# Kernel tuning notes

Measured on AMD Instinct MI355X. Metric: run time of the kernel, lower is better.

Reference implementation:

```python
import jax, jax.numpy as jnp
import numpy as np

N_HEAD = 8
LN_EPS = 1e-5


def _ln(z, g, b):
    m = jnp.mean(z, axis=-1, keepdims=True)
    v = jnp.var(z, axis=-1, keepdims=True)
    return (z - m) / jnp.sqrt(v + LN_EPS) * g + b


def setup_inputs() -> dict:
    key = jax.random.key(0)
    ks = jax.random.split(key, 20)
    B, N, H, F = 4, 256, 128, 512
    p = {}
    p["x"] = jax.random.normal(ks[0], (B, N, H), dtype=jnp.float32)
    p["e"] = jax.random.normal(ks[1], (B, N, N, H), dtype=jnp.float32)
    p["attention_mask"] = jnp.zeros((B, N_HEAD, N, N), dtype=jnp.float32)
    s = 0.02
    p["Wq"] = jax.random.normal(ks[2], (H, H)) * s; p["bq"] = jnp.zeros((H,))
    p["Wk"] = jax.random.normal(ks[3], (H, H)) * s; p["bk"] = jnp.zeros((H,))
    p["Wv"] = jax.random.normal(ks[4], (H, H)) * s; p["bv"] = jnp.zeros((H,))
    p["We"] = jax.random.normal(ks[5], (H, H)) * s; p["be"] = jnp.zeros((H,))
    p["Woh"] = jax.random.normal(ks[6], (H, H)) * s; p["boh"] = jnp.zeros((H,))
    p["Woe"] = jax.random.normal(ks[7], (H, H)) * s; p["boe"] = jnp.zeros((H,))
    p["Wf1x"] = jax.random.normal(ks[8], (H, F)) * s; p["bf1x"] = jnp.zeros((F,))
    p["Wf2x"] = jax.random.normal(ks[9], (F, H)) * s; p["bf2x"] = jnp.zeros((H,))
    p["Wf1e"] = jax.random.normal(ks[10], (H, F)) * s; p["bf1e"] = jnp.zeros((F,))
    p["Wf2e"] = jax.random.normal(ks[11], (F, H)) * s; p["bf2e"] = jnp.zeros((H,))
    p["g1x"] = jnp.ones((H,)); p["b1x"] = jnp.zeros((H,))
    p["g1e"] = jnp.ones((H,)); p["b1e"] = jnp.zeros((H,))
    return p


def reference(x, e, attention_mask, Wq, bq, Wk, bk, Wv, bv, We, be,
              Woh, boh, Woe, boe, Wf1x, bf1x, Wf2x, bf2x,
              Wf1e, bf1e, Wf2e, bf2e, g1x, b1x, g1e, b1e):
    B, N, H = x.shape
    h = N_HEAD
    d = H // h
    # projections; NOTE: V uses the K projection (faithful to original bug)
    Qx = (x @ Wq + bq).reshape(B, N, h, d).transpose(0, 2, 1, 3)   # (B,h,N,d)
    Kx = (x @ Wk + bk).reshape(B, N, h, d).transpose(0, 2, 1, 3)
    Vx = (x @ Wk + bk).reshape(B, N, h, d).transpose(0, 2, 1, 3)
    Ee = (e @ We + be).reshape(B, N, N, h, d).transpose(0, 3, 1, 2, 4)  # (B,h,N,N,d)
    scale = 1.0 / np.sqrt(d).astype(np.float32)
    inter = Qx[:, :, :, None, :] * Kx[:, :, None, :, :] * Ee * scale   # (B,h,N,N,d)
    scores = jax.nn.softmax(attention_mask + inter.sum(-1), axis=-1)   # (B,h,N,N)
    e_attn = inter.transpose(0, 2, 3, 1, 4).reshape(B, N, N, H) @ Woe + boe
    att = jnp.einsum('bhij,bhjd->bhid', scores, Vx)
    x_attn = att.transpose(0, 2, 1, 3).reshape(B, N, H) @ Woh + boh
    # residual + layernorm (original 'layer' path reuses normalization1_* twice)
    x1 = _ln(x_attn + x, g1x, b1x)
    e1 = _ln(e_attn + e, g1e, b1e)
    x_ff = jax.nn.relu(x1 @ Wf1x + bf1x) @ Wf2x + bf2x
    e_ff = jax.nn.relu(e1 @ Wf1e + bf1e) @ Wf2e + bf2e
    x2 = _ln(x_ff + x1, g1x, b1x)
    e2 = _ln(e_ff + e1, g1e, b1e)
    return x2, e2
```

## Files before the change

kernel.cpp:

```cpp
#include <hip/hip_runtime.h>
#include <math.h>

#define NSEQ 256
#define HD 128
#define FD 512
#define NHD 8
#define LNEPS 1e-5f

typedef __attribute__((ext_vector_type(8))) short bf16x8;
typedef __attribute__((ext_vector_type(4))) float f32x4;

__device__ __forceinline__ unsigned short f2bf(float x) {
  union { float f; unsigned int u; } v; v.f = x;
  unsigned int r = v.u + 0x7fffu + ((v.u >> 16) & 1u);
  return (unsigned short)(r >> 16);
}

__device__ __forceinline__ float bf2f(unsigned short u) {
  union { float f; unsigned int v; } cv; cv.v = ((unsigned int)u) << 16;
  return cv.f;
}

__global__ void prep_weights(
    const float* __restrict__ W1x, const float* __restrict__ W2x,
    const float* __restrict__ W1e, const float* __restrict__ W2e,
    unsigned short* __restrict__ W1Tx, unsigned short* __restrict__ W2Tx,
    unsigned short* __restrict__ W1Fe, unsigned short* __restrict__ W2Fe) {
  int t = blockIdx.x * 256 + threadIdx.x;
  int tot = gridDim.x * 256;
  for (int idx = t; idx < FD * HD; idx += tot) {
    int n = idx >> 7, k = idx & (HD - 1);
    float v = W1x[k * FD + n];
    W1Tx[idx] = f2bf(v);
    float ve = W1e[k * FD + n];
    int dst = ((((n >> 4) * 4 + (k >> 5)) * 64) + ((k >> 3) & 3) * 16 + (n & 15)) * 8 + (k & 7);
    W1Fe[dst] = f2bf(ve);
  }
  for (int idx = t; idx < HD * FD; idx += tot) {
    int n = idx >> 9, k = idx & (FD - 1);
    float v = W2x[k * HD + n];
    W2Tx[idx] = f2bf(v);
    float ve = W2e[k * HD + n];
    int dst = ((((n >> 4) * 16 + (k >> 5)) * 64) + ((k >> 3) & 3) * 16 + (n & 15)) * 8 + (k & 7);
    W2Fe[dst] = f2bf(ve);
  }
}

__global__ __launch_bounds__(128) void qk_proj(const float* __restrict__ x,
    const float* __restrict__ Wq, const float* __restrict__ bq,
    const float* __restrict__ Wk, const float* __restrict__ bk,
    float* __restrict__ Qs, float* __restrict__ Kp) {
  int row = blockIdx.x;
  int c = threadIdx.x;
  __shared__ float xl[HD];
  xl[c] = x[row * HD + c];
  __syncthreads();
  float aq = bq[c], ak = bk[c];
  #pragma unroll 8
  for (int k = 0; k < HD; ++k) {
    float xv = xl[k];
    aq = fmaf(xv, Wq[k * HD + c], aq);
    ak = fmaf(xv, Wk[k * HD + c], ak);
  }
  Qs[row * HD + c] = aq * 0.25f;
  Kp[row * HD + c] = ak;
}

__global__ __launch_bounds__(256) void edge_attn(
    const float* __restrict__ e,
    const float* __restrict__ We, const float* __restrict__ be,
    const float* __restrict__ Woe, const float* __restrict__ boe,
    const float* __restrict__ Qs, const float* __restrict__ Kp,
    const float* __restrict__ g1e, const float* __restrict__ b1e,
    float* __restrict__ Sout, float* __restrict__ e1out) {
  const int gid = blockIdx.x;
  const int jt = gid & 3, i = (gid >> 2) & (NSEQ - 1), b = gid >> 10;
  const int j0 = jt * 64;
  const int t = threadIdx.x;
  const int w = t >> 6, l = t & 63;
  const int wr = w >> 1, wc = w & 1;
  const int l15 = l & 15, lg = l >> 4;

  __shared__ unsigned short eL[64 * 128];
  __shared__ unsigned short kL[64 * 136];
  __shared__ float qL[HD], beL[HD], boeL[HD], gL[HD], bbL[HD];
  __shared__ float redS[64][2], redQ[64][2];

  if (t < HD) {
    qL[t]   = Qs[(b * NSEQ + i) * HD + t];
    beL[t]  = be[t];
    boeL[t] = boe[t];
    gL[t]   = g1e[t];
    bbL[t]  = b1e[t];
  }
  const int ebase = ((b * NSEQ + i) * NSEQ + j0) * HD;
  for (int v = t; v < 64 * 16; v += 256) {
    int r = v >> 4, c8 = (v & 15) << 3;
    const float* se = &e[ebase + r * HD + c8];
    float4 e0 = *(const float4*)se;
    float4 e1v = *(const float4*)(se + 4);
    union { bf16x8 v8; unsigned short u[8]; } pk;
    pk.u[0] = f2bf(e0.x); pk.u[1] = f2bf(e0.y); pk.u[2] = f2bf(e0.z); pk.u[3] = f2bf(e0.w);
    pk.u[4] = f2bf(e1v.x); pk.u[5] = f2bf(e1v.y); pk.u[6] = f2bf(e1v.z); pk.u[7] = f2bf(e1v.w);
    *(bf16x8*)&eL[r * HD + (c8 ^ ((r & 7) << 3))] = pk.v8;
    const float* sk = &Kp[(b * NSEQ + j0 + r) * HD + c8];
    float4 k0 = *(const float4*)sk;
    float4 k1 = *(const float4*)(sk + 4);
    pk.u[0] = f2bf(k0.x); pk.u[1] = f2bf(k0.y); pk.u[2] = f2bf(k0.z); pk.u[3] = f2bf(k0.w);
    pk.u[4] = f2bf(k1.x); pk.u[5] = f2bf(k1.y); pk.u[6] = f2bf(k1.z); pk.u[7] = f2bf(k1.w);
    *(bf16x8*)&kL[r * 136 + c8] = pk.v8;
  }
  __syncthreads();

  f32x4 acc1[2][4];
  #pragma unroll
  for (int tm = 0; tm < 2; ++tm)
    #pragma unroll
    for (int tn = 0; tn < 4; ++tn) {
      float bv = beL[wc * 64 + tn * 16 + l15];
      acc1[tm][tn] = (f32x4){bv, bv, bv, bv};
    }
  #pragma unroll
  for (int ks = 0; ks < 4; ++ks) {
    bf16x8 af[2], bfr[4];
    #pragma unroll
    for (int tm = 0; tm < 2; ++tm) {
      int mrow = wr * 32 + tm * 16 + l15;
      af[tm] = *(const bf16x8*)&eL[mrow * HD + ((ks * 32 + lg * 8) ^ ((mrow & 7) << 3))];
    }
    #pragma unroll
    for (int tn = 0; tn < 4; ++tn) {
      int n = wc * 64 + tn * 16 + l15;
      const float* wp = &We[(ks * 32 + lg * 8) * HD + n];
      union { bf16x8 v8; unsigned short u[8]; } pk;
      #pragma unroll
      for (int ii = 0; ii < 8; ++ii) pk.u[ii] = f2bf(wp[ii * HD]);
      bfr[tn] = pk.v8;
    }
    #pragma unroll
    for (int tm = 0; tm < 2; ++tm)
      #pragma unroll
      for (int tn = 0; tn < 4; ++tn)
        acc1[tm][tn] = __builtin_amdgcn_mfma_f32_16x16x32_bf16(af[tm], bfr[tn], acc1[tm][tn], 0, 0, 0);
  }

  #pragma unroll
  for (int tm = 0; tm < 2; ++tm)
    #pragma unroll
    for (int tn = 0; tn < 4; ++tn) {
      int c = wc * 64 + tn * 16 + l15;
      float qv = qL[c];
      f32x4 p;
      #pragma unroll
      for (int ii = 0; ii < 4; ++ii) {
        int r = wr * 32 + tm * 16 + lg * 4 + ii;
        p[ii] = acc1[tm][tn][ii] * qv * bf2f(kL[r * 136 + c]);
      }
      acc1[tm][tn] = p;
      float h0 = p[0], h1 = p[1], h2 = p[2], h3 = p[3];
      #pragma unroll
      for (int off = 1; off < 16; off <<= 1) {
        h0 += __shfl_xor(h0, off); h1 += __shfl_xor(h1, off);
        h2 += __shfl_xor(h2, off); h3 += __shfl_xor(h3, off);
      }
      if (l15 < 4) {
        float val = l15 == 0 ? h0 : l15 == 1 ? h1 : l15 == 2 ? h2 : h3;
        int r = wr * 32 + tm * 16 + lg * 4 + l15;
        Sout[((b * NHD + (wc * 4 + tn)) * NSEQ + i) * NSEQ + j0 + r] = val;
      }
    }
  __syncthreads();

  #pragma unroll
  for (int tm = 0; tm < 2; ++tm)
    #pragma unroll
    for (int tn = 0; tn < 4; ++tn) {
      int c = wc * 64 + tn * 16 + l15;
      #pragma unroll
      for (int ii = 0; ii < 4; ++ii) {
        int r = wr * 32 + tm * 16 + lg * 4 + ii;
        eL[r * HD + (c ^ ((r & 7) << 3))] = f2bf(acc1[tm][tn][ii]);
      }
    }
  __syncthreads();

  f32x4 acc2[2][4];
  #pragma unroll
  for (int tm = 0; tm < 2; ++tm)
    #pragma unroll
    for (int tn = 0; tn < 4; ++tn) {
      float bv = boeL[wc * 64 + tn * 16 + l15];
      acc2[tm][tn] = (f32x4){bv, bv, bv, bv};
    }
  #pragma unroll
  for (int ks = 0; ks < 4; ++ks) {
    bf16x8 af[2], bfr[4];
    #pragma unroll
    for (int tm = 0; tm < 2; ++tm) {
      int mrow = wr * 32 + tm * 16 + l15;
      af[tm] = *(const bf16x8*)&eL[mrow * HD + ((ks * 32 + lg * 8) ^ ((mrow & 7) << 3))];
    }
    #pragma unroll
    for (int tn = 0; tn < 4; ++tn) {
      int n = wc * 64 + tn * 16 + l15;
      const float* wp = &Woe[(ks * 32 + lg * 8) * HD + n];
      union { bf16x8 v8; unsigned short u[8]; } pk;
      #pragma unroll
      for (int ii = 0; ii < 8; ++ii) pk.u[ii] = f2bf(wp[ii * HD]);
      bfr[tn] = pk.v8;
    }
    #pragma unroll
    for (int tm = 0; tm < 2; ++tm)
      #pragma unroll
      for (int tn = 0; tn < 4; ++tn)
        acc2[tm][tn] = __builtin_amdgcn_mfma_f32_16x16x32_bf16(af[tm], bfr[tn], acc2[tm][tn], 0, 0, 0);
  }

  #pragma unroll
  for (int tm = 0; tm < 2; ++tm) {
    #pragma unroll
    for (int tn = 0; tn < 4; ++tn) {
      int c = wc * 64 + tn * 16 + l15;
      #pragma unroll
      for (int ii = 0; ii < 4; ++ii) {
        int r = wr * 32 + tm * 16 + lg * 4 + ii;
        acc2[tm][tn][ii] += e[ebase + r * HD + c];
      }
    }
    #pragma unroll
    for (int ii = 0; ii < 4; ++ii) {
      float s  = acc2[tm][0][ii] + acc2[tm][1][ii] + acc2[tm][2][ii] + acc2[tm][3][ii];
      float sq = acc2[tm][0][ii] * acc2[tm][0][ii] + acc2[tm][1][ii] * acc2[tm][1][ii]
               + acc2[tm][2][ii] * acc2[tm][2][ii] + acc2[tm][3][ii] * acc2[tm][3][ii];
      #pragma unroll
      for (int off = 1; off < 16; off <<= 1) {
        s += __shfl_xor(s, off); sq += __shfl_xor(sq, off);
      }
      if (l15 == 0) {
        int r = wr * 32 + tm * 16 + lg * 4 + ii;
        redS[r][wc] = s; redQ[r][wc] = sq;
      }
    }
  }
  __syncthreads();

  #pragma unroll
  for (int tm = 0; tm < 2; ++tm) {
    float mrow[4], rsrow[4];
    #pragma unroll
    for (int ii = 0; ii < 4; ++ii) {
      int r = wr * 32 + tm * 16 + lg * 4 + ii;
      float s = redS[r][0] + redS[r][1];
      float sq = redQ[r][0] + redQ[r][1];
      float m = s * (1.f / HD);
      float var = sq * (1.f / HD) - m * m;
      mrow[ii] = m; rsrow[ii] = rsqrtf(var + LNEPS);
    }
    #pragma unroll
    for (int tn = 0; tn < 4; ++tn) {
      int c = wc * 64 + tn * 16 + l15;
      float gv = gL[c], bv = bbL[c];
      #pragma unroll
      for (int ii = 0; ii < 4; ++ii) {
        int r = wr * 32 + tm * 16 + lg * 4 + ii;
        e1out[ebase + r * HD + c] = (acc2[tm][tn][ii] - mrow[ii]) * rsrow[ii] * gv + bv;
      }
    }
  }
}

__global__ __launch_bounds__(256) void softmax_k(float* __restrict__ S,
    const float* __restrict__ mask) {
  int row = blockIdx.x;
  int t = threadIdx.x;
  int idx = row * NSEQ + t;
  float v = S[idx] + mask[idx];
  float m = v;
  #pragma unroll
  for (int off = 1; off < 64; off <<= 1) m = fmaxf(m, __shfl_xor(m, off));
  __shared__ float wbuf[8];
  if ((t & 63) == 0) wbuf[t >> 6] = m;
  __syncthreads();
  m = fmaxf(fmaxf(wbuf[0], wbuf[1]), fmaxf(wbuf[2], wbuf[3]));
  float ex = __expf(v - m);
  float s = ex;
  #pragma unroll
  for (int off = 1; off < 64; off <<= 1) s += __shfl_xor(s, off);
  __syncthreads();
  if ((t & 63) == 0) wbuf[4 + (t >> 6)] = s;
  __syncthreads();
  s = wbuf[4] + wbuf[5] + wbuf[6] + wbuf[7];
  S[idx] = ex / s;
}

__global__ __launch_bounds__(128) void x_attn_ln(
    const float* __restrict__ x, const float* __restrict__ scores,
    const float* __restrict__ Kp,
    const float* __restrict__ Woh, const float* __restrict__ boh,
    const float* __restrict__ g1x, const float* __restrict__ b1x,
    float* __restrict__ x1out) {
  int bi = blockIdx.x; int b = bi >> 8; int i = bi & 255;
  int c = threadIdx.x;
  __shared__ float sL[NHD * NSEQ];
  __shared__ float attL[HD];
  __shared__ float rbuf[4];

  for (int v = c; v < NHD * NSEQ; v += 128) {
    int h = v >> 8, j = v & 255;
    sL[v] = scores[((b * NHD + h) * NSEQ + i) * NSEQ + j];
  }
  __syncthreads();
  int h = c >> 4;
  float att = 0.f;
  for (int j = 0; j < NSEQ; ++j)
    att = fmaf(sL[h * NSEQ + j], Kp[(b * NSEQ + j) * HD + c], att);
  attL[c] = att;
  __syncthreads();
  float o = boh[c];
  for (int k = 0; k < HD; ++k) o = fmaf(attL[k], Woh[k * HD + c], o);
  o += x[bi * HD + c];
  float s = o, s2 = o * o;
  #pragma unroll
  for (int off = 1; off < 64; off <<= 1) { s += __shfl_xor(s, off); s2 += __shfl_xor(s2, off); }
  if ((c & 63) == 0) { rbuf[(c >> 6) * 2] = s; rbuf[(c >> 6) * 2 + 1] = s2; }
  __syncthreads();
  s = rbuf[0] + rbuf[2]; s2 = rbuf[1] + rbuf[3];
  float m = s * (1.f / HD);
  float var = s2 * (1.f / HD) - m * m;
  x1out[bi * HD + c] = (o - m) * rsqrtf(var + LNEPS) * g1x[c] + b1x[c];
}

__global__ __launch_bounds__(256) void ffn_mfma(
    const float* in1,
    const unsigned short* __restrict__ W1T, const float* __restrict__ b1,
    const unsigned short* __restrict__ W2T, const float* __restrict__ b2,
    const float* __restrict__ g, const float* __restrict__ bb,
    float* out2) {
  const int row0 = blockIdx.x * 64;
  const int t = threadIdx.x;
  const int w = t >> 6, l = t & 63;
  const int wr = w >> 1, wc = w & 1;
  const int l15 = l & 15, lg = l >> 4;

  __shared__ __align__(16) char smem[34816];
  unsigned short* aL = (unsigned short*)smem;
  unsigned short* hL = (unsigned short*)(smem + 16384);
  float* b1L = (float*)(smem + 32768);
  float* epi = (float*)smem;

  for (int v = t; v < 64 * 16; v += 256) {
    int r = v >> 4, c8 = (v & 15) << 3;
    const float* src = &in1[(row0 + r) * HD + c8];
    float4 f0 = *(const float4*)src;
    float4 f1 = *(const float4*)(src + 4);
    union { bf16x8 v8; unsigned short u[8]; } pk;
    pk.u[0] = f2bf(f0.x); pk.u[1] = f2bf(f0.y); pk.u[2] = f2bf(f0.z); pk.u[3] = f2bf(f0.w);
    pk.u[4] = f2bf(f1.x); pk.u[5] = f2bf(f1.y); pk.u[6] = f2bf(f1.z); pk.u[7] = f2bf(f1.w);
    *(bf16x8*)&aL[r * HD + (c8 ^ ((r & 7) << 3))] = pk.v8;
  }
  for (int v = t; v < FD; v += 256) b1L[v] = b1[v];
  __syncthreads();

  f32x4 acc2[2][4];
  #pragma unroll
  for (int tm = 0; tm < 2; ++tm)
    #pragma unroll
    for (int tn = 0; tn < 4; ++tn) acc2[tm][tn] = (f32x4){0.f, 0.f, 0.f, 0.f};

  for (int fc = 0; fc < 4; ++fc) {
    f32x4 acc1[2][4];
    #pragma unroll
    for (int tm = 0; tm < 2; ++tm)
      #pragma unroll
      for (int tn = 0; tn < 4; ++tn) acc1[tm][tn] = (f32x4){0.f, 0.f, 0.f, 0.f};
    #pragma unroll
    for (int ks = 0; ks < 4; ++ks) {
      bf16x8 af[2], bfr[4];
      #pragma unroll
      for (int tm = 0; tm < 2; ++tm) {
        int mrow = wr * 32 + tm * 16 + l15;
        af[tm] = *(const bf16x8*)&aL[mrow * HD + ((ks * 32 + lg * 8) ^ ((mrow & 7) << 3))];
      }
      #pragma unroll
      for (int tn = 0; tn < 4; ++tn) {
        int n = fc * 128 + wc * 64 + tn * 16 + l15;
        bfr[tn] = *(const bf16x8*)&W1T[n * HD + ks * 32 + lg * 8];
      }
      #pragma unroll
      for (int tm = 0; tm < 2; ++tm)
        #pragma unroll
        for (int tn = 0; tn < 4; ++tn)
          acc1[tm][tn] = __builtin_amdgcn_mfma_f32_16x16x32_bf16(af[tm], bfr[tn], acc1[tm][tn], 0, 0, 0);
    }
    __syncthreads();
    #pragma unroll
    for (int tm = 0; tm < 2; ++tm)
      #pragma unroll
      for (int tn = 0; tn < 4; ++tn) {
        int col = wc * 64 + tn * 16 + l15;
        float bias = b1L[fc * 128 + col];
        #pragma unroll
        for (int ii = 0; ii < 4; ++ii) {
          int r = wr * 32 + tm * 16 + lg * 4 + ii;
          float hv = fmaxf(acc1[tm][tn][ii] + bias, 0.f);
          hL[r * HD + (col ^ ((r & 7) << 3))] = f2bf(hv);
        }
      }
    __syncthreads();
    #pragma unroll
    for (int ks = 0; ks < 4; ++ks) {
      bf16x8 af[2], bfr[4];
      #pragma unroll
      for (int tm = 0; tm < 2; ++tm) {
        int mrow = wr * 32 + tm * 16 + l15;
        af[tm] = *(const bf16x8*)&hL[mrow * HD + ((ks * 32 + lg * 8) ^ ((mrow & 7) << 3))];
      }
      #pragma unroll
      for (int tn = 0; tn < 4; ++tn) {
        int n = wc * 64 + tn * 16 + l15;
        bfr[tn] = *(const bf16x8*)&W2T[n * FD + fc * 128 + ks * 32 + lg * 8];
      }
      #pragma unroll
      for (int tm = 0; tm < 2; ++tm)
        #pragma unroll
        for (int tn = 0; tn < 4; ++tn)
          acc2[tm][tn] = __builtin_amdgcn_mfma_f32_16x16x32_bf16(af[tm], bfr[tn], acc2[tm][tn], 0, 0, 0);
    }
  }

  float res[2][4][4];
  #pragma unroll
  for (int tm = 0; tm < 2; ++tm)
    #pragma unroll
    for (int tn = 0; tn < 4; ++tn) {
      int col = wc * 64 + tn * 16 + l15;
      #pragma unroll
      for (int ii = 0; ii < 4; ++ii) {
        int r = wr * 32 + tm * 16 + lg * 4 + ii;
        res[tm][tn][ii] = bf2f(aL[r * HD + (col ^ ((r & 7) << 3))]);
      }
    }
  __syncthreads();

  #pragma unroll
  for (int tm = 0; tm < 2; ++tm)
    #pragma unroll
    for (int tn = 0; tn < 4; ++tn) {
      int col = wc * 64 + tn * 16 + l15;
      float bias = b2[col];
      #pragma unroll
      for (int ii = 0; ii < 4; ++ii) {
        int r = wr * 32 + tm * 16 + lg * 4 + ii;
        epi[r * 132 + col] = acc2[tm][tn][ii] + bias + res[tm][tn][ii];
      }
    }
  __syncthreads();
  {
    int r = t >> 2, sgi = t & 3;
    const float* rowp = &epi[r * 132 + sgi * 32];
    float sum = 0.f, sq = 0.f;
    #pragma unroll
    for (int u = 0; u < 32; u += 4) {
      float4 v4 = *(const float4*)&rowp[u];
      sum += v4.x + v4.y + v4.z + v4.w;
      sq  += v4.x * v4.x + v4.y * v4.y + v4.z * v4.z + v4.w * v4.w;
    }
    sum += __shfl_xor(sum, 1); sq += __shfl_xor(sq, 1);
    sum += __shfl_xor(sum, 2); sq += __shfl_xor(sq, 2);
    float m = sum * (1.f / HD);
    float var = sq * (1.f / HD) - m * m;
    float rs = rsqrtf(var + LNEPS);
    #pragma unroll
    for (int u = 0; u < 32; u += 4) {
      float4 v4 = *(const float4*)&rowp[u];
      int cb = sgi * 32 + u;
      float4 o;
      o.x = (v4.x - m) * rs * g[cb + 0] + bb[cb + 0];
      o.y = (v4.y - m) * rs * g[cb + 1] + bb[cb + 1];
      o.z = (v4.z - m) * rs * g[cb + 2] + bb[cb + 2];
      o.w = (v4.w - m) * rs * g[cb + 3] + bb[cb + 3];
      *(float4*)&out2[(row0 + r) * HD + cb] = o;
    }
  }
}

__global__ __launch_bounds__(256) void ffn_mfma_e(
    const float* in1,
    const unsigned short* __restrict__ W1F, const float* __restrict__ b1,
    const unsigned short* __restrict__ W2F, const float* __restrict__ b2,
    const float* __restrict__ g, const float* __restrict__ bb,
    float* out2) {
  const int t = threadIdx.x;
  const int w = t >> 6, l = t & 63;
  const int wr = w >> 1, wc = w & 1;
  const int l15 = l & 15, lg = l >> 4;
  const int rowbase = blockIdx.x * 256;

  __shared__ __align__(16) char smem[35840];
  unsigned short* aL = (unsigned short*)smem;
  unsigned short* hL = (unsigned short*)(smem + 16384);
  float* b1L  = (float*)(smem + 32768);
  float* redS = (float*)(smem + 34816);
  float* redQ = (float*)(smem + 35328);

  for (int v = t; v < FD; v += 256) b1L[v] = b1[v];

  for (int ch = 0; ch < 4; ++ch) {
    const int row0 = rowbase + ch * 64;
    __syncthreads();

    for (int v = t; v < 64 * 16; v += 256) {
      int r = v >> 4, c8 = (v & 15) << 3;
      const float* src = &in1[(row0 + r) * HD + c8];
      float4 f0 = *(const float4*)src;
      float4 f1 = *(const float4*)(src + 4);
      union { bf16x8 v8; unsigned short u[8]; } pk;
      pk.u[0] = f2bf(f0.x); pk.u[1] = f2bf(f0.y); pk.u[2] = f2bf(f0.z); pk.u[3] = f2bf(f0.w);
      pk.u[4] = f2bf(f1.x); pk.u[5] = f2bf(f1.y); pk.u[6] = f2bf(f1.z); pk.u[7] = f2bf(f1.w);
      *(bf16x8*)&aL[r * HD + (c8 ^ ((r & 7) << 3))] = pk.v8;
    }
    __syncthreads();

    f32x4 acc2[2][4];
    #pragma unroll
    for (int tm = 0; tm < 2; ++tm)
      #pragma unroll
      for (int tn = 0; tn < 4; ++tn) acc2[tm][tn] = (f32x4){0.f, 0.f, 0.f, 0.f};

    for (int fc = 0; fc < 4; ++fc) {
      f32x4 acc1[2][4];
      #pragma unroll
      for (int tm = 0; tm < 2; ++tm)
        #pragma unroll
        for (int tn = 0; tn < 4; ++tn) acc1[tm][tn] = (f32x4){0.f, 0.f, 0.f, 0.f};
      #pragma unroll
      for (int ks = 0; ks < 4; ++ks) {
        bf16x8 af[2], bfr[4];
        #pragma unroll
        for (int tm = 0; tm < 2; ++tm) {
          int mrow = wr * 32 + tm * 16 + l15;
          af[tm] = *(const bf16x8*)&aL[mrow * HD + ((ks * 32 + lg * 8) ^ ((mrow & 7) << 3))];
        }
        #pragma unroll
        for (int tn = 0; tn < 4; ++tn) {
          int nt = fc * 8 + wc * 4 + tn;
          bfr[tn] = *(const bf16x8*)&W1F[(((nt * 4 + ks) * 64) + l) * 8];
        }
        #pragma unroll
        for (int tm = 0; tm < 2; ++tm)
          #pragma unroll
          for (int tn = 0; tn < 4; ++tn)
            acc1[tm][tn] = __builtin_amdgcn_mfma_f32_16x16x32_bf16(af[tm], bfr[tn], acc1[tm][tn], 0, 0, 0);
      }
      __syncthreads();
      #pragma unroll
      for (int tm = 0; tm < 2; ++tm)
        #pragma unroll
        for (int tn = 0; tn < 4; ++tn) {
          int col = wc * 64 + tn * 16 + l15;
          float bias = b1L[fc * 128 + col];
          #pragma unroll
          for (int ii = 0; ii < 4; ++ii) {
            int r = wr * 32 + tm * 16 + lg * 4 + ii;
            float hv = fmaxf(acc1[tm][tn][ii] + bias, 0.f);
            hL[r * HD + (col ^ ((r & 7) << 3))] = f2bf(hv);
          }
        }
      __syncthreads();
      #pragma unroll
      for (int ks = 0; ks < 4; ++ks) {
        bf16x8 af[2], bfr[4];
        #pragma unroll
        for (int tm = 0; tm < 2; ++tm) {
          int mrow = wr * 32 + tm * 16 + l15;
          af[tm] = *(const bf16x8*)&hL[mrow * HD + ((ks * 32 + lg * 8) ^ ((mrow & 7) << 3))];
        }
        #pragma unroll
        for (int tn = 0; tn < 4; ++tn) {
          int nt = wc * 4 + tn;
          int ksg = fc * 4 + ks;
          bfr[tn] = *(const bf16x8*)&W2F[(((nt * 16 + ksg) * 64) + l) * 8];
        }
        #pragma unroll
        for (int tm = 0; tm < 2; ++tm)
          #pragma unroll
          for (int tn = 0; tn < 4; ++tn)
            acc2[tm][tn] = __builtin_amdgcn_mfma_f32_16x16x32_bf16(af[tm], bfr[tn], acc2[tm][tn], 0, 0, 0);
      }
    }

    #pragma unroll
    for (int tm = 0; tm < 2; ++tm) {
      #pragma unroll
      for (int tn = 0; tn < 4; ++tn) {
        int col = wc * 64 + tn * 16 + l15;
        float bias = b2[col];
        #pragma unroll
        for (int ii = 0; ii < 4; ++ii) {
          int r = wr * 32 + tm * 16 + lg * 4 + ii;
          acc2[tm][tn][ii] += bias + bf2f(aL[r * HD + (col ^ ((r & 7) << 3))]);
        }
      }
      #pragma unroll
      for (int ii = 0; ii < 4; ++ii) {
        float s  = acc2[tm][0][ii] + acc2[tm][1][ii] + acc2[tm][2][ii] + acc2[tm][3][ii];
        float sq = acc2[tm][0][ii] * acc2[tm][0][ii] + acc2[tm][1][ii] * acc2[tm][1][ii]
                 + acc2[tm][2][ii] * acc2[tm][2][ii] + acc2[tm][3][ii] * acc2[tm][3][ii];
        #pragma unroll
        for (int off = 1; off < 16; off <<= 1) {
          s += __shfl_xor(s, off); sq += __shfl_xor(sq, off);
        }
        if (l15 == 0) {
          int r = wr * 32 + tm * 16 + lg * 4 + ii;
          redS[r * 2 + wc] = s; redQ[r * 2 + wc] = sq;
        }
      }
    }
    __syncthreads();

    #pragma unroll
    for (int tm = 0; tm < 2; ++tm) {
      float mrow[4], rsrow[4];
      #pragma unroll
      for (int ii = 0; ii < 4; ++ii) {
        int r = wr * 32 + tm * 16 + lg * 4 + ii;
        float s = redS[r * 2] + redS[r * 2 + 1];
        float sq = redQ[r * 2] + redQ[r * 2 + 1];
        float m = s * (1.f / HD);
        float var = sq * (1.f / HD) - m * m;
        mrow[ii] = m; rsrow[ii] = rsqrtf(var + LNEPS);
      }
      #pragma unroll
      for (int tn = 0; tn < 4; ++tn) {
        int col = wc * 64 + tn * 16 + l15;
        float gv = g[col], bv = bb[col];
        #pragma unroll
        for (int ii = 0; ii < 4; ++ii) {
          int r = wr * 32 + tm * 16 + lg * 4 + ii;
          out2[(row0 + r) * HD + col] = (acc2[tm][tn][ii] - mrow[ii]) * rsrow[ii] * gv + bv;
        }
      }
    }
  }
}

extern "C" void kernel_launch(void* const* d_in, const int* in_sizes, int n_in,
                              void* d_out, int out_size, void* d_ws, size_t ws_size,
                              hipStream_t stream) {
  const float* x    = (const float*)d_in[0];
  const float* e    = (const float*)d_in[1];
  const float* mask = (const float*)d_in[2];
  const float* Wq   = (const float*)d_in[3];
  const float* bq   = (const float*)d_in[4];
  const float* Wk   = (const float*)d_in[5];
  const float* bk   = (const float*)d_in[6];
  const float* We   = (const float*)d_in[9];
  const float* be   = (const float*)d_in[10];
  const float* Woh  = (const float*)d_in[11];
  const float* boh  = (const float*)d_in[12];
  const float* Woe  = (const float*)d_in[13];
  const float* boe  = (const float*)d_in[14];
  const float* Wf1x = (const float*)d_in[15];
  const float* bf1x = (const float*)d_in[16];
  const float* Wf2x = (const float*)d_in[17];
  const float* bf2x = (const float*)d_in[18];
  const float* Wf1e = (const float*)d_in[19];
  const float* bf1e = (const float*)d_in[20];
  const float* Wf2e = (const float*)d_in[21];
  const float* bf2e = (const float*)d_in[22];
  const float* g1x  = (const float*)d_in[23];
  const float* b1x  = (const float*)d_in[24];
  const float* g1e  = (const float*)d_in[25];
  const float* b1e  = (const float*)d_in[26];

  float* xout = (float*)d_out;
  float* eout = (float*)d_out + 131072;

  char* ws = (char*)d_ws;
  unsigned short* W1Fe = (unsigned short*)(ws);
  unsigned short* W2Fe = (unsigned short*)(ws + 131072);
  unsigned short* W1Tx = (unsigned short*)(ws + 262144);
  unsigned short* W2Tx = (unsigned short*)(ws + 393216);
  float* Qs  = (float*)(ws + 524288);
  float* Kp  = (float*)(ws + 1048576);
  float* x1b = (float*)(ws + 1572864);
  float* S   = (float*)(ws + 2097152);

  prep_weights<<<64, 256, 0, stream>>>(Wf1x, Wf2x, Wf1e, Wf2e, W1Tx, W2Tx, W1Fe, W2Fe);
  qk_proj<<<1024, 128, 0, stream>>>(x, Wq, bq, Wk, bk, Qs, Kp);
  edge_attn<<<4096, 256, 0, stream>>>(e, We, be, Woe, boe, Qs, Kp, g1e, b1e, S, eout);
  softmax_k<<<8192, 256, 0, stream>>>(S, mask);
  x_attn_ln<<<1024, 128, 0, stream>>>(x, S, Kp, Woh, boh, g1x, b1x, x1b);
  ffn_mfma<<<16, 256, 0, stream>>>(x1b, W1Tx, bf1x, W2Tx, bf2x, g1x, b1x, xout);
  ffn_mfma_e<<<1024, 256, 0, stream>>>(eout, W1Fe, bf1e, W2Fe, bf2e, g1e, b1e, eout);
}
```

Before: 408.0 us.

## Fuse edge FFN and second layernorm into the edge attention kernel

The edge FFN (two bf16 MFMA GEMMs with ReLU, residual and layernorm) now runs inside the edge attention kernel. The e1 tile stays in LDS as bf16, and the K tile buffer is reused for the hidden activations. This removes one 64 MB write and one 64 MB read of the intermediate e1 tensor plus a separate launch. In exchange each block holds more LDS and registers, which may lower occupancy of the fused kernel.

```diff
diff --git a/kernel.cpp b/kernel.cpp
--- a/kernel.cpp
+++ b/kernel.cpp
@@ -30,16 +30,14 @@
   int tot = gridDim.x * 256;
   for (int idx = t; idx < FD * HD; idx += tot) {
     int n = idx >> 7, k = idx & (HD - 1);
-    float v = W1x[k * FD + n];
-    W1Tx[idx] = f2bf(v);
+    W1Tx[idx] = f2bf(W1x[k * FD + n]);
     float ve = W1e[k * FD + n];
     int dst = ((((n >> 4) * 4 + (k >> 5)) * 64) + ((k >> 3) & 3) * 16 + (n & 15)) * 8 + (k & 7);
     W1Fe[dst] = f2bf(ve);
   }
   for (int idx = t; idx < HD * FD; idx += tot) {
     int n = idx >> 9, k = idx & (FD - 1);
-    float v = W2x[k * HD + n];
-    W2Tx[idx] = f2bf(v);
+    W2Tx[idx] = f2bf(W2x[k * HD + n]);
     float ve = W2e[k * HD + n];
     int dst = ((((n >> 4) * 16 + (k >> 5)) * 64) + ((k >> 3) & 3) * 16 + (n & 15)) * 8 + (k & 7);
     W2Fe[dst] = f2bf(ve);
@@ -66,13 +64,15 @@
   Kp[row * HD + c] = ak;
 }
 
-__global__ __launch_bounds__(256) void edge_attn(
+__global__ __launch_bounds__(256) void edge_attn_ffn(
     const float* __restrict__ e,
     const float* __restrict__ We, const float* __restrict__ be,
     const float* __restrict__ Woe, const float* __restrict__ boe,
     const float* __restrict__ Qs, const float* __restrict__ Kp,
     const float* __restrict__ g1e, const float* __restrict__ b1e,
-    float* __restrict__ Sout, float* __restrict__ e1out) {
+    const unsigned short* __restrict__ W1F, const float* __restrict__ b1f,
+    const unsigned short* __restrict__ W2F, const float* __restrict__ b2f,
+    float* __restrict__ Sout, float* __restrict__ e2out) {
   const int gid = blockIdx.x;
   const int jt = gid & 3, i = (gid >> 2) & (NSEQ - 1), b = gid >> 10;
   const int j0 = jt * 64;
@@ -84,7 +84,9 @@
   __shared__ unsigned short eL[64 * 128];
   __shared__ unsigned short kL[64 * 136];
   __shared__ float qL[HD], beL[HD], boeL[HD], gL[HD], bbL[HD];
+  __shared__ float b1L[FD];
   __shared__ float redS[64][2], redQ[64][2];
+  unsigned short* hLr = kL;
 
   if (t < HD) {
     qL[t]   = Qs[(b * NSEQ + i) * HD + t];
@@ -93,6 +95,7 @@
     gL[t]   = g1e[t];
     bbL[t]  = b1e[t];
   }
+  for (int v = t; v < FD; v += 256) b1L[v] = b1f[v];
   const int ebase = ((b * NSEQ + i) * NSEQ + j0) * HD;
   for (int v = t; v < 64 * 16; v += 256) {
     int r = v >> 4, c8 = (v & 15) << 3;
@@ -263,7 +266,130 @@
       #pragma unroll
       for (int ii = 0; ii < 4; ++ii) {
         int r = wr * 32 + tm * 16 + lg * 4 + ii;
-        e1out[ebase + r * HD + c] = (acc2[tm][tn][ii] - mrow[ii]) * rsrow[ii] * gv + bv;
+        float e1v = (acc2[tm][tn][ii] - mrow[ii]) * rsrow[ii] * gv + bv;
+        eL[r * HD + (c ^ ((r & 7) << 3))] = f2bf(e1v);
+      }
+    }
+  }
+  __syncthreads();
+
+  f32x4 accF[2][4];
+  #pragma unroll
+  for (int tm = 0; tm < 2; ++tm)
+    #pragma unroll
+    for (int tn = 0; tn < 4; ++tn) accF[tm][tn] = (f32x4){0.f, 0.f, 0.f, 0.f};
+
+  for (int fc = 0; fc < 4; ++fc) {
+    f32x4 accH[2][4];
+    #pragma unroll
+    for (int tm = 0; tm < 2; ++tm)
+      #pragma unroll
+      for (int tn = 0; tn < 4; ++tn) accH[tm][tn] = (f32x4){0.f, 0.f, 0.f, 0.f};
+    #pragma unroll
+    for (int ks = 0; ks < 4; ++ks) {
+      bf16x8 af[2], bfr[4];
+      #pragma unroll
+      for (int tm = 0; tm < 2; ++tm) {
+        int mrow = wr * 32 + tm * 16 + l15;
+        af[tm] = *(const bf16x8*)&eL[mrow * HD + ((ks * 32 + lg * 8) ^ ((mrow & 7) << 3))];
+      }
+      #pragma unroll
+      for (int tn = 0; tn < 4; ++tn) {
+        int nt = fc * 8 + wc * 4 + tn;
+        bfr[tn] = *(const bf16x8*)&W1F[(((nt * 4 + ks) * 64) + l) * 8];
+      }
+      #pragma unroll
+      for (int tm = 0; tm < 2; ++tm)
+        #pragma unroll
+        for (int tn = 0; tn < 4; ++tn)
+          accH[tm][tn] = __builtin_amdgcn_mfma_f32_16x16x32_bf16(af[tm], bfr[tn], accH[tm][tn], 0, 0, 0);
+    }
+    __syncthreads();
+    #pragma unroll
+    for (int tm = 0; tm < 2; ++tm)
+      #pragma unroll
+      for (int tn = 0; tn < 4; ++tn) {
+        int col = wc * 64 + tn * 16 + l15;
+        float bias = b1L[fc * 128 + col];
+        #pragma unroll
+        for (int ii = 0; ii < 4; ++ii) {
+          int r = wr * 32 + tm * 16 + lg * 4 + ii;
+          float hv = fmaxf(accH[tm][tn][ii] + bias, 0.f);
+          hLr[r * HD + (col ^ ((r & 7) << 3))] = f2bf(hv);
+        }
+      }
+    __syncthreads();
+    #pragma unroll
+    for (int ks = 0; ks < 4; ++ks) {
+      bf16x8 af[2], bfr[4];
+      #pragma unroll
+      for (int tm = 0; tm < 2; ++tm) {
+        int mrow = wr * 32 + tm * 16 + l15;
+        af[tm] = *(const bf16x8*)&hLr[mrow * HD + ((ks * 32 + lg * 8) ^ ((mrow & 7) << 3))];
+      }
+      #pragma unroll
+      for (int tn = 0; tn < 4; ++tn) {
+        int nt = wc * 4 + tn;
+        int ksg = fc * 4 + ks;
+        bfr[tn] = *(const bf16x8*)&W2F[(((nt * 16 + ksg) * 64) + l) * 8];
+      }
+      #pragma unroll
+      for (int tm = 0; tm < 2; ++tm)
+        #pragma unroll
+        for (int tn = 0; tn < 4; ++tn)
+          accF[tm][tn] = __builtin_amdgcn_mfma_f32_16x16x32_bf16(af[tm], bfr[tn], accF[tm][tn], 0, 0, 0);
+    }
+  }
+
+  #pragma unroll
+  for (int tm = 0; tm < 2; ++tm) {
+    #pragma unroll
+    for (int tn = 0; tn < 4; ++tn) {
+      int col = wc * 64 + tn * 16 + l15;
+      float bias = b2f[col];
+      #pragma unroll
+      for (int ii = 0; ii < 4; ++ii) {
+        int r = wr * 32 + tm * 16 + lg * 4 + ii;
+        accF[tm][tn][ii] += bias + bf2f(eL[r * HD + (col ^ ((r & 7) << 3))]);
+      }
+    }
+    #pragma unroll
+    for (int ii = 0; ii < 4; ++ii) {
+      float s  = accF[tm][0][ii] + accF[tm][1][ii] + accF[tm][2][ii] + accF[tm][3][ii];
+      float sq = accF[tm][0][ii] * accF[tm][0][ii] + accF[tm][1][ii] * accF[tm][1][ii]
+               + accF[tm][2][ii] * accF[tm][2][ii] + accF[tm][3][ii] * accF[tm][3][ii];
+      #pragma unroll
+      for (int off = 1; off < 16; off <<= 1) {
+        s += __shfl_xor(s, off); sq += __shfl_xor(sq, off);
+      }
+      if (l15 == 0) {
+        int r = wr * 32 + tm * 16 + lg * 4 + ii;
+        redS[r][wc] = s; redQ[r][wc] = sq;
+      }
+    }
+  }
+  __syncthreads();
+
+  #pragma unroll
+  for (int tm = 0; tm < 2; ++tm) {
+    float mrow[4], rsrow[4];
+    #pragma unroll
+    for (int ii = 0; ii < 4; ++ii) {
+      int r = wr * 32 + tm * 16 + lg * 4 + ii;
+      float s = redS[r][0] + redS[r][1];
+      float sq = redQ[r][0] + redQ[r][1];
+      float m = s * (1.f / HD);
+      float var = sq * (1.f / HD) - m * m;
+      mrow[ii] = m; rsrow[ii] = rsqrtf(var + LNEPS);
+    }
+    #pragma unroll
+    for (int tn = 0; tn < 4; ++tn) {
+      int c = wc * 64 + tn * 16 + l15;
+      float gv = gL[c], bv = bbL[c];
+      #pragma unroll
+      for (int ii = 0; ii < 4; ++ii) {
+        int r = wr * 32 + tm * 16 + lg * 4 + ii;
+        e2out[ebase + r * HD + c] = (accF[tm][tn][ii] - mrow[ii]) * rsrow[ii] * gv + bv;
       }
     }
   }
@@ -480,166 +606,6 @@
       o.z = (v4.z - m) * rs * g[cb + 2] + bb[cb + 2];
       o.w = (v4.w - m) * rs * g[cb + 3] + bb[cb + 3];
       *(float4*)&out2[(row0 + r) * HD + cb] = o;
-    }
-  }
-}
-
-__global__ __launch_bounds__(256) void ffn_mfma_e(
-    const float* in1,
-    const unsigned short* __restrict__ W1F, const float* __restrict__ b1,
-    const unsigned short* __restrict__ W2F, const float* __restrict__ b2,
-    const float* __restrict__ g, const float* __restrict__ bb,
-    float* out2) {
-  const int t = threadIdx.x;
-  const int w = t >> 6, l = t & 63;
-  const int wr = w >> 1, wc = w & 1;
-  const int l15 = l & 15, lg = l >> 4;
-  const int rowbase = blockIdx.x * 256;
-
-  __shared__ __align__(16) char smem[35840];
-  unsigned short* aL = (unsigned short*)smem;
-  unsigned short* hL = (unsigned short*)(smem + 16384);
-  float* b1L  = (float*)(smem + 32768);
-  float* redS = (float*)(smem + 34816);
-  float* redQ = (float*)(smem + 35328);
-
-  for (int v = t; v < FD; v += 256) b1L[v] = b1[v];
-
-  for (int ch = 0; ch < 4; ++ch) {
-    const int row0 = rowbase + ch * 64;
-    __syncthreads();
-
-    for (int v = t; v < 64 * 16; v += 256) {
-      int r = v >> 4, c8 = (v & 15) << 3;
-      const float* src = &in1[(row0 + r) * HD + c8];
-      float4 f0 = *(const float4*)src;
-      float4 f1 = *(const float4*)(src + 4);
-      union { bf16x8 v8; unsigned short u[8]; } pk;
-      pk.u[0] = f2bf(f0.x); pk.u[1] = f2bf(f0.y); pk.u[2] = f2bf(f0.z); pk.u[3] = f2bf(f0.w);
-      pk.u[4] = f2bf(f1.x); pk.u[5] = f2bf(f1.y); pk.u[6] = f2bf(f1.z); pk.u[7] = f2bf(f1.w);
-      *(bf16x8*)&aL[r * HD + (c8 ^ ((r & 7) << 3))] = pk.v8;
-    }
-    __syncthreads();
-
-    f32x4 acc2[2][4];
-    #pragma unroll
-    for (int tm = 0; tm < 2; ++tm)
-      #pragma unroll
-      for (int tn = 0; tn < 4; ++tn) acc2[tm][tn] = (f32x4){0.f, 0.f, 0.f, 0.f};
-
-    for (int fc = 0; fc < 4; ++fc) {
-      f32x4 acc1[2][4];
-      #pragma unroll
-      for (int tm = 0; tm < 2; ++tm)
-        #pragma unroll
-        for (int tn = 0; tn < 4; ++tn) acc1[tm][tn] = (f32x4){0.f, 0.f, 0.f, 0.f};
-      #pragma unroll
-      for (int ks = 0; ks < 4; ++ks) {
-        bf16x8 af[2], bfr[4];
-        #pragma unroll
-        for (int tm = 0; tm < 2; ++tm) {
-          int mrow = wr * 32 + tm * 16 + l15;
-          af[tm] = *(const bf16x8*)&aL[mrow * HD + ((ks * 32 + lg * 8) ^ ((mrow & 7) << 3))];
-        }
-        #pragma unroll
-        for (int tn = 0; tn < 4; ++tn) {
-          int nt = fc * 8 + wc * 4 + tn;
-          bfr[tn] = *(const bf16x8*)&W1F[(((nt * 4 + ks) * 64) + l) * 8];
-        }
-        #pragma unroll
-        for (int tm = 0; tm < 2; ++tm)
-          #pragma unroll
-          for (int tn = 0; tn < 4; ++tn)
-            acc1[tm][tn] = __builtin_amdgcn_mfma_f32_16x16x32_bf16(af[tm], bfr[tn], acc1[tm][tn], 0, 0, 0);
-      }
-      __syncthreads();
-      #pragma unroll
-      for (int tm = 0; tm < 2; ++tm)
-        #pragma unroll
-        for (int tn = 0; tn < 4; ++tn) {
-          int col = wc * 64 + tn * 16 + l15;
-          float bias = b1L[fc * 128 + col];
-          #pragma unroll
-          for (int ii = 0; ii < 4; ++ii) {
-            int r = wr * 32 + tm * 16 + lg * 4 + ii;
-            float hv = fmaxf(acc1[tm][tn][ii] + bias, 0.f);
-            hL[r * HD + (col ^ ((r & 7) << 3))] = f2bf(hv);
-          }
-        }
-      __syncthreads();
-      #pragma unroll
-      for (int ks = 0; ks < 4; ++ks) {
-        bf16x8 af[2], bfr[4];
-        #pragma unroll
-        for (int tm = 0; tm < 2; ++tm) {
-          int mrow = wr * 32 + tm * 16 + l15;
-          af[tm] = *(const bf16x8*)&hL[mrow * HD + ((ks * 32 + lg * 8) ^ ((mrow & 7) << 3))];
-        }
-        #pragma unroll
-        for (int tn = 0; tn < 4; ++tn) {
-          int nt = wc * 4 + tn;
-          int ksg = fc * 4 + ks;
-          bfr[tn] = *(const bf16x8*)&W2F[(((nt * 16 + ksg) * 64) + l) * 8];
-        }
-        #pragma unroll
-        for (int tm = 0; tm < 2; ++tm)
-          #pragma unroll
-          for (int tn = 0; tn < 4; ++tn)
-            acc2[tm][tn] = __builtin_amdgcn_mfma_f32_16x16x32_bf16(af[tm], bfr[tn], acc2[tm][tn], 0, 0, 0);
-      }
-    }
-
-    #pragma unroll
-    for (int tm = 0; tm < 2; ++tm) {
-      #pragma unroll
-      for (int tn = 0; tn < 4; ++tn) {
-        int col = wc * 64 + tn * 16 + l15;
-        float bias = b2[col];
-        #pragma unroll
-        for (int ii = 0; ii < 4; ++ii) {
-          int r = wr * 32 + tm * 16 + lg * 4 + ii;
-          acc2[tm][tn][ii] += bias + bf2f(aL[r * HD + (col ^ ((r & 7) << 3))]);
-        }
-      }
-      #pragma unroll
-      for (int ii = 0; ii < 4; ++ii) {
-        float s  = acc2[tm][0][ii] + acc2[tm][1][ii] + acc2[tm][2][ii] + acc2[tm][3][ii];
-        float sq = acc2[tm][0][ii] * acc2[tm][0][ii] + acc2[tm][1][ii] * acc2[tm][1][ii]
-                 + acc2[tm][2][ii] * acc2[tm][2][ii] + acc2[tm][3][ii] * acc2[tm][3][ii];
-        #pragma unroll
-        for (int off = 1; off < 16; off <<= 1) {
-          s += __shfl_xor(s, off); sq += __shfl_xor(sq, off);
-        }
-        if (l15 == 0) {
-          int r = wr * 32 + tm * 16 + lg * 4 + ii;
-          redS[r * 2 + wc] = s; redQ[r * 2 + wc] = sq;
-        }
-      }
-    }
-    __syncthreads();
-
-    #pragma unroll
-    for (int tm = 0; tm < 2; ++tm) {
-      float mrow[4], rsrow[4];
-      #pragma unroll
-      for (int ii = 0; ii < 4; ++ii) {
-        int r = wr * 32 + tm * 16 + lg * 4 + ii;
-        float s = redS[r * 2] + redS[r * 2 + 1];
-        float sq = redQ[r * 2] + redQ[r * 2 + 1];
-        float m = s * (1.f / HD);
-        float var = sq * (1.f / HD) - m * m;
-        mrow[ii] = m; rsrow[ii] = rsqrtf(var + LNEPS);
-      }
-      #pragma unroll
-      for (int tn = 0; tn < 4; ++tn) {
-        int col = wc * 64 + tn * 16 + l15;
-        float gv = g[col], bv = bb[col];
-        #pragma unroll
-        for (int ii = 0; ii < 4; ++ii) {
-          int r = wr * 32 + tm * 16 + lg * 4 + ii;
-          out2[(row0 + r) * HD + col] = (acc2[tm][tn][ii] - mrow[ii]) * rsrow[ii] * gv + bv;
-        }
-      }
     }
   }
 }
@@ -688,9 +654,9 @@
 
   prep_weights<<<64, 256, 0, stream>>>(Wf1x, Wf2x, Wf1e, Wf2e, W1Tx, W2Tx, W1Fe, W2Fe);
   qk_proj<<<1024, 128, 0, stream>>>(x, Wq, bq, Wk, bk, Qs, Kp);
-  edge_attn<<<4096, 256, 0, stream>>>(e, We, be, Woe, boe, Qs, Kp, g1e, b1e, S, eout);
+  edge_attn_ffn<<<4096, 256, 0, stream>>>(e, We, be, Woe, boe, Qs, Kp, g1e, b1e,
+                                          W1Fe, bf1e, W2Fe, bf2e, S, eout);
   softmax_k<<<8192, 256, 0, stream>>>(S, mask);
   x_attn_ln<<<1024, 128, 0, stream>>>(x, S, Kp, Woh, boh, g1x, b1x, x1b);
   ffn_mfma<<<16, 256, 0, stream>>>(x1b, W1Tx, bf1x, W2Tx, bf2x, g1x, b1x, xout);
-  ffn_mfma_e<<<1024, 256, 0, stream>>>(eout, W1Fe, bf1e, W2Fe, bf2e, g1e, b1e, eout);
-}
+}
```

New measurement: 492.5 us. 20.7% more time.
